# Performance work log

Measured on AMD Instinct MI355X. Metric: run time of the kernel, lower is better.

## Reference

```python
import jax, jax.numpy as jnp
import numpy as np

N = 200000      # total nodes
B = 1024        # graphs
D = 256         # node_dim
OUT = 256       # out_dim


def setup_inputs() -> dict:
    key = jax.random.key(0)
    ks = jax.random.split(key, 16)
    x = jax.random.normal(ks[0], (N, D), dtype=jnp.float32)
    # sorted segment ids covering all B graphs (no empty segments)
    extra = jax.random.randint(ks[1], (N - B,), 0, B)
    batch = jnp.sort(jnp.concatenate([jnp.arange(B, dtype=jnp.int32), extra.astype(jnp.int32)]))
    # one-hot node type mask [N, 3]
    types = jax.random.randint(ks[2], (N,), 0, 3)
    node_type_mask = jax.nn.one_hot(types, 3, dtype=jnp.int32)
    s = 1.0 / np.sqrt(D)
    # attn_weight: Linear(D, D//2) -> Tanh -> Linear(D//2, 1)
    aw1 = jax.random.uniform(ks[3], (D, D // 2), jnp.float32, -s, s)
    ab1 = jnp.zeros((D // 2,), jnp.float32)
    aw2 = jax.random.uniform(ks[4], (D // 2, 1), jnp.float32, -s, s)
    ab2 = jnp.zeros((1,), jnp.float32)
    # three typed transforms Linear(D, D)
    we = jax.random.uniform(ks[5], (D, D), jnp.float32, -s, s)
    be = jnp.zeros((D,), jnp.float32)
    wv = jax.random.uniform(ks[6], (D, D), jnp.float32, -s, s)
    bv = jnp.zeros((D,), jnp.float32)
    wp = jax.random.uniform(ks[7], (D, D), jnp.float32, -s, s)
    bp = jnp.zeros((D,), jnp.float32)
    # readout MLP: Linear(3D, 2*OUT) -> SiLU -> (Dropout eval) -> Linear(2*OUT, OUT)
    w1 = jax.random.uniform(ks[8], (3 * D, 2 * OUT), jnp.float32, -1.0 / np.sqrt(3 * D), 1.0 / np.sqrt(3 * D))
    b1 = jnp.zeros((2 * OUT,), jnp.float32)
    w2 = jax.random.uniform(ks[9], (2 * OUT, OUT), jnp.float32, -1.0 / np.sqrt(2 * OUT), 1.0 / np.sqrt(2 * OUT))
    b2 = jnp.zeros((OUT,), jnp.float32)
    return dict(x=x, batch=batch, node_type_mask=node_type_mask, num_segments=B,
                aw1=aw1, ab1=ab1, aw2=aw2, ab2=ab2, we=we, be=be, wv=wv, bv=bv,
                wp=wp, bp=bp, w1=w1, b1=b1, w2=w2, b2=b2)


def reference(x, batch, node_type_mask, num_segments,
              aw1, ab1, aw2, ab2, we, be, wv, bv, wp, bp, w1, b1, w2, b2):
    nseg = int(num_segments)
    # global_mean_pool
    counts = jax.ops.segment_sum(jnp.ones((x.shape[0],), x.dtype), batch, num_segments=nseg)
    mean_pool = jax.ops.segment_sum(x, batch, num_segments=nseg) / counts[:, None]
    # attention scores + segment softmax
    scores = jnp.tanh(x @ aw1 + ab1) @ aw2 + ab2            # [N, 1]
    s = scores[:, 0]
    m = jax.ops.segment_max(s, batch, num_segments=nseg)    # [B]
    e = jnp.exp(s - m[batch])
    z = jax.ops.segment_sum(e, batch, num_segments=nseg)
    attn = e / z[batch]                                     # [N]
    attn_pool = jax.ops.segment_sum(x * attn[:, None], batch, num_segments=nseg)
    # typed physical pooling (node_type_mask path)
    mask = node_type_mask.astype(x.dtype)
    typed_x = (mask[:, 0:1] * (x @ we + be)
               + mask[:, 1:2] * (x @ wv + bv)
               + mask[:, 2:3] * (x @ wp + bp))
    phys_pool = jax.ops.segment_sum(typed_x, batch, num_segments=nseg)
    combined = jnp.concatenate([mean_pool, attn_pool, phys_pool], axis=-1)  # [B, 3D]
    h = jax.nn.silu(combined @ w1 + b1)                     # dropout = identity (eval)
    return h @ w2 + b2                                      # [B, OUT]
```

## Files before the change

### kernel.cpp

```cpp
#include <hip/hip_runtime.h>

typedef float  f32x4  __attribute__((ext_vector_type(4)));
typedef short  s16x8  __attribute__((ext_vector_type(8)));
typedef short  s16x4  __attribute__((ext_vector_type(4)));

__device__ __forceinline__ short f2bf(float f) {
  unsigned u = __float_as_uint(f);
  u += 0x7fffu + ((u >> 16) & 1u);
  return (short)(u >> 16);
}
__device__ __forceinline__ float bf2f(unsigned short us) {
  return __uint_as_float(((unsigned)us) << 16);
}
__device__ __forceinline__ float tanh_fast(float x) {
  const float e = __expf(2.0f * x);
  return 1.0f - 2.0f / (e + 1.0f);
}

__global__ __launch_bounds__(256) void k_cvtw(
    const float* __restrict__ aw1, const float* __restrict__ we, const float* __restrict__ wv,
    const float* __restrict__ wp, const float* __restrict__ w1, const float* __restrict__ w2,
    unsigned short* __restrict__ Awt, unsigned short* __restrict__ Wpt,
    unsigned short* __restrict__ W1t, unsigned short* __restrict__ W2t,
    float* __restrict__ Z) {
  const int b = blockIdx.x, tid = threadIdx.x;
  if (b >= 184) {
    const int idx = b - 184;
    f32x4* Z4 = reinterpret_cast<f32x4*>(Z);
    const f32x4 z4 = {0.f, 0.f, 0.f, 0.f};
#pragma unroll
    for (int j = 0; j < 4; ++j) {
      const int o = idx * 1024 + j * 256 + tid;
      if (o < 263168) Z4[o] = z4;
    }
    return;
  }
  __shared__ short T[64][65];
  const float* src; unsigned short* dst;
  int N, ds, off, t;
  if (b < 8)        { src = aw1; dst = Awt; N = 128; ds = 256; off = 0;   t = b; }
  else if (b < 24)  { src = we;  dst = Wpt; N = 256; ds = 768; off = 0;   t = b - 8; }
  else if (b < 40)  { src = wv;  dst = Wpt; N = 256; ds = 768; off = 256; t = b - 24; }
  else if (b < 56)  { src = wp;  dst = Wpt; N = 256; ds = 768; off = 512; t = b - 40; }
  else if (b < 152) { src = w1;  dst = W1t; N = 512; ds = 768; off = 0;   t = b - 56; }
  else              { src = w2;  dst = W2t; N = 256; ds = 512; off = 0;   t = b - 152; }
  const int ntx = N >> 6;
  const int kt = t / ntx;
  const int k0 = kt * 64, n0 = (t - kt * ntx) * 64;
  const int rl = tid >> 6, cl = tid & 63;
#pragma unroll
  for (int i = 0; i < 16; ++i)
    T[cl][i * 4 + rl] = f2bf(src[(size_t)(k0 + i * 4 + rl) * N + n0 + cl]);
  __syncthreads();
#pragma unroll
  for (int i = 0; i < 16; ++i)
    dst[(size_t)(n0 + i * 4 + rl) * ds + off + k0 + cl] = (unsigned short)T[i * 4 + rl][cl];
}

__global__ __launch_bounds__(256, 2) void k_score_pool(
    const float* __restrict__ x, const int* __restrict__ batch, const int* __restrict__ mask,
    const unsigned short* __restrict__ Awt, const float* __restrict__ ab1,
    const float* __restrict__ aw2, const float* __restrict__ ab2,
    float* __restrict__ P, float* __restrict__ EX, float* __restrict__ ZC,
    int nnodes) {
  __shared__ __align__(16) short xs[2][32][264];
  __shared__ __align__(16) short xsB[2][8192];
  __shared__ __align__(16) float sred[2][4][32];
  __shared__ __align__(16) short em[16][40];
  __shared__ int st_all[320];

  const int tid  = threadIdx.x;
  const int lane = tid & 63;
  const int w    = tid >> 6;
  const int quad = lane >> 4;
  const int l15  = lane & 15;

  s16x8 bfrag[8][2];
  float ab1v[2], aw2v[2];
#pragma unroll
  for (int ct = 0; ct < 2; ++ct) {
    const int col = w * 32 + ct * 16 + l15;
    ab1v[ct] = ab1[col];
    aw2v[ct] = aw2[col];
    const s16x8* bp = reinterpret_cast<const s16x8*>(Awt + (size_t)col * 256);
#pragma unroll
    for (int kt = 0; kt < 8; ++kt) bfrag[kt][ct] = bp[kt * 4 + quad];
  }
  const float ab2v = ab2[0];

  const int tiles = nnodes >> 5;
  const int t_beg = (int)(((long long)blockIdx.x * tiles) / (long long)gridDim.x);
  const int t_end = (int)(((long long)(blockIdx.x + 1) * tiles) / (long long)gridDim.x);
  if (t_beg >= t_end) return;
  const int nt = t_end - t_beg;

  {
    const int nodes0 = t_beg * 32, nblk = nt * 32;
    for (int i = tid; i < nblk; i += 256) {
      const int g = nodes0 + i;
      st_all[i] = batch[g] * 4 + mask[g * 3 + 1] + 2 * mask[g * 3 + 2];
    }
    for (int i = tid; i < 640; i += 256) (&em[0][0])[i] = 0;
  }

  f32x4 stg[8];
  auto load_regs = [&](int tile) {
    const f32x4* xp = reinterpret_cast<const f32x4*>(x + (size_t)tile * 8192);
#pragma unroll
    for (int i = 0; i < 8; ++i) stg[i] = xp[(8 * w + i) * 64 + lane];
  };
  auto cvt_write = [&](int bb) {
    s16x4 xv[8];
#pragma unroll
    for (int i = 0; i < 8; ++i) {
      xv[i][0] = f2bf(stg[i][0]); xv[i][1] = f2bf(stg[i][1]);
      xv[i][2] = f2bf(stg[i][2]); xv[i][3] = f2bf(stg[i][3]);
    }
#pragma unroll
    for (int i = 0; i < 8; ++i)
      *reinterpret_cast<s16x4*>(&xs[bb][8 * w + i][lane * 4]) = xv[i];
    const int gb = (lane >> 2) * 4 + w;
    const int lb = (lane & 3) * 4;
#pragma unroll
    for (int q = 0; q < 4; ++q) {
      s16x8 v;
#pragma unroll
      for (int j = 0; j < 8; ++j) v[j] = xv[j][q];
      *reinterpret_cast<s16x8*>(&xsB[bb][(gb * 16 + lb + q) * 8]) = v;
    }
  };

  load_regs(t_beg);
  cvt_write(0);
  __syncthreads();

  const f32x4 zero4 = {0.f, 0.f, 0.f, 0.f};
  f32x4 accB[4] = {zero4, zero4, zero4, zero4};
  float zA = 0.f, c0A = 0.f, c1A = 0.f, c2A = 0.f;
  int cur = -1;

  auto flushB = [&]() {
#pragma unroll
    for (int c = 0; c < 4; ++c) {
      const int col = w * 64 + c * 16 + l15;
      if (quad == 0) {
        atomicAdd(&EX[cur * 256 + col], accB[c][0] + accB[c][1]);
        atomicAdd(&P[cur * 768 + col], accB[c][2]);
        atomicAdd(&P[cur * 768 + 256 + col], accB[c][3]);
      } else if (quad == 1) {
        atomicAdd(&P[cur * 768 + 512 + col], accB[c][0]);
      }
      accB[c] = zero4;
    }
    if (w == 0) {
      if (lane < 4) {
        const float v = (lane == 0) ? zA : ((lane == 1) ? c0A : ((lane == 2) ? c1A : c2A));
        atomicAdd(&ZC[cur * 4 + lane], v);
      }
      zA = c0A = c1A = c2A = 0.f;
    }
  };

  auto POOL = [&](int base, int par, s16x8 f0, s16x8 f1, s16x8 f2, s16x8 f3) {
    float e_f = 0.f;
    int myt = 3;
    if (lane < 32) {
      const float s = ab2v + sred[par][0][lane] + sred[par][1][lane] +
                      sred[par][2][lane] + sred[par][3][lane];
      e_f = __expf(s);
      const unsigned short hi = (unsigned short)f2bf(e_f);
      const unsigned short lo = (unsigned short)f2bf(e_f - bf2f(hi));
      myt = st_all[base + lane] & 3;
      em[0][lane] = (short)hi;
      em[1][lane] = (short)lo;
      em[2][lane] = (myt == 0) ? (short)0x3f80 : (short)0;
      em[3][lane] = (myt == 1) ? (short)0x3f80 : (short)0;
      em[4][lane] = (myt == 2) ? (short)0x3f80 : (short)0;
    }
    const int myseg = (lane < 32) ? (st_all[base + lane] >> 2) : 0x7fffffff;
    s16x8 emf = *reinterpret_cast<const s16x8*>(&em[l15][quad * 8]);

    int n0 = 0;
    while (n0 < 32) {
      const int seg = st_all[base + n0] >> 2;
      const unsigned long long diff = __ballot(lane < 32 && myseg != seg) >> n0;
      const int n1 = (diff == 0) ? 32 : n0 + (int)__builtin_ctzll(diff);
      if (seg != cur) { if (cur >= 0) flushB(); cur = seg; }
      s16x8 af;
      const int kb = quad * 8;
#pragma unroll
      for (int j = 0; j < 8; ++j) {
        const int k = kb + j;
        af[j] = (k >= n0 && k < n1) ? emf[j] : (short)0;
      }
      accB[0] = __builtin_amdgcn_mfma_f32_16x16x32_bf16(af, f0, accB[0], 0, 0, 0);
      accB[1] = __builtin_amdgcn_mfma_f32_16x16x32_bf16(af, f1, accB[1], 0, 0, 0);
      accB[2] = __builtin_amdgcn_mfma_f32_16x16x32_bf16(af, f2, accB[2], 0, 0, 0);
      accB[3] = __builtin_amdgcn_mfma_f32_16x16x32_bf16(af, f3, accB[3], 0, 0, 0);
      if (w == 0) {
        const bool inrun = (lane >= n0 && lane < n1 && lane < 32);
        float ee = inrun ? e_f : 0.f;
#pragma unroll
        for (int off = 1; off < 32; off <<= 1) ee += __shfl_xor(ee, off);
        const unsigned long long b0 = __ballot(inrun && myt == 0);
        const unsigned long long b1 = __ballot(inrun && myt == 1);
        const unsigned long long b2 = __ballot(inrun && myt == 2);
        zA  += ee;
        c0A += (float)__popcll(b0);
        c1A += (float)__popcll(b1);
        c2A += (float)__popcll(b2);
      }
      n0 = n1;
    }
  };

  s16x8 bfBp0, bfBp1, bfBp2, bfBp3;

  for (int lt = 0; lt < nt; ++lt) {
    const int p    = lt & 1;
    const int tile = t_beg + lt;
    const bool more = (lt + 1 < nt);
    if (more) load_regs(tile + 1);

#pragma unroll
    for (int ng = 0; ng < 2; ++ng) {
      s16x8 af[8];
#pragma unroll
      for (int kt = 0; kt < 8; ++kt)
        af[kt] = *reinterpret_cast<const s16x8*>(&xs[p][16 * ng + l15][kt * 32 + quad * 8]);
      float part[4] = {0.f, 0.f, 0.f, 0.f};
#pragma unroll
      for (int ct = 0; ct < 2; ++ct) {
        f32x4 acc = {0.f, 0.f, 0.f, 0.f};
#pragma unroll
        for (int kt = 0; kt < 8; ++kt)
          acc = __builtin_amdgcn_mfma_f32_16x16x32_bf16(af[kt], bfrag[kt][ct], acc, 0, 0, 0);
#pragma unroll
        for (int r = 0; r < 4; ++r)
          part[r] += tanh_fast(acc[r] + ab1v[ct]) * aw2v[ct];
      }
#pragma unroll
      for (int off = 1; off < 16; off <<= 1) {
#pragma unroll
        for (int r = 0; r < 4; ++r) part[r] += __shfl_xor(part[r], off);
      }
      if (l15 == 0) {
#pragma unroll
        for (int r = 0; r < 4; ++r) sred[p][w][16 * ng + quad * 4 + r] = part[r];
      }
    }

    const s16x8 bfBn0 = *reinterpret_cast<const s16x8*>(
        &xsB[p][(((w * 4 + 0) * 4 + quad) * 16 + l15) * 8]);
    const s16x8 bfBn1 = *reinterpret_cast<const s16x8*>(
        &xsB[p][(((w * 4 + 1) * 4 + quad) * 16 + l15) * 8]);
    const s16x8 bfBn2 = *reinterpret_cast<const s16x8*>(
        &xsB[p][(((w * 4 + 2) * 4 + quad) * 16 + l15) * 8]);
    const s16x8 bfBn3 = *reinterpret_cast<const s16x8*>(
        &xsB[p][(((w * 4 + 3) * 4 + quad) * 16 + l15) * 8]);

    if (lt > 0) POOL((lt - 1) * 32, p ^ 1, bfBp0, bfBp1, bfBp2, bfBp3);

    if (more) cvt_write(p ^ 1);

    __syncthreads();
    bfBp0 = bfBn0; bfBp1 = bfBn1; bfBp2 = bfBn2; bfBp3 = bfBn3;
  }

  POOL((nt - 1) * 32, (nt - 1) & 1, bfBp0, bfBp1, bfBp2, bfBp3);
  if (cur >= 0) flushB();
}

__global__ __launch_bounds__(256) void k_phys(
    const float* __restrict__ P, const unsigned short* __restrict__ Wpt,
    const float* __restrict__ be, const float* __restrict__ bv, const float* __restrict__ bp,
    const float* __restrict__ ZC, float* __restrict__ PH) {
  __shared__ __align__(16) short as16[16][776];
  const int tid = threadIdx.x, lane = tid & 63, w = tid >> 6;
  const int quad = lane >> 4, l15 = lane & 15;
  const int rowbase = blockIdx.x * 16;
  const int col = blockIdx.y * 64 + w * 16 + l15;

  s16x8 bfr[24];
  const s16x8* bpf = reinterpret_cast<const s16x8*>(Wpt + (size_t)col * 768);
#pragma unroll
  for (int kt = 0; kt < 24; ++kt) bfr[kt] = bpf[kt * 4 + quad];

  const f32x4* ap = reinterpret_cast<const f32x4*>(P + (size_t)rowbase * 768);
#pragma unroll
  for (int i = 0; i < 12; ++i) {
    const int ci = tid + 256 * i;
    f32x4 v = ap[ci];
    const int row = ci / 192, c4 = (ci % 192) * 4;
    s16x4 b; b[0] = f2bf(v[0]); b[1] = f2bf(v[1]); b[2] = f2bf(v[2]); b[3] = f2bf(v[3]);
    *reinterpret_cast<s16x4*>(&as16[row][c4]) = b;
  }
  __syncthreads();

  f32x4 acc = {0.f, 0.f, 0.f, 0.f};
#pragma unroll
  for (int kt = 0; kt < 24; ++kt) {
    s16x8 af = *reinterpret_cast<const s16x8*>(&as16[l15][kt * 32 + quad * 8]);
    acc = __builtin_amdgcn_mfma_f32_16x16x32_bf16(af, bfr[kt], acc, 0, 0, 0);
  }
  const float ben = be[col], bvn = bv[col], bpn = bp[col];
#pragma unroll
  for (int r = 0; r < 4; ++r) {
    const int row = rowbase + quad * 4 + r;
    const float v = acc[r] + ZC[row * 4 + 1] * ben + ZC[row * 4 + 2] * bvn + ZC[row * 4 + 3] * bpn;
    PH[(size_t)row * 256 + col] = v;
  }
}

__global__ __launch_bounds__(256) void k_mlp1(
    const float* __restrict__ P, const float* __restrict__ EX,
    const float* __restrict__ ZC, const float* __restrict__ PH,
    const unsigned short* __restrict__ W1t, const float* __restrict__ b1,
    float* __restrict__ H) {
  __shared__ __align__(16) short as16[16][776];
  const int tid = threadIdx.x, lane = tid & 63, w = tid >> 6;
  const int quad = lane >> 4, l15 = lane & 15;
  const int rowbase = blockIdx.x * 16;
  const int col = blockIdx.y * 64 + w * 16 + l15;

  s16x8 bfr[24];
  const s16x8* bpf = reinterpret_cast<const s16x8*>(W1t + (size_t)col * 768);
#pragma unroll
  for (int kt = 0; kt < 24; ++kt) bfr[kt] = bpf[kt * 4 + quad];

#pragma unroll 4
  for (int r = 0; r < 16; ++r) {
    const int row = rowbase + r;
    const float z   = ZC[row * 4 + 0];
    const float cnt = ZC[row * 4 + 1] + ZC[row * 4 + 2] + ZC[row * 4 + 3];
    const float mp  = (P[(size_t)row * 768 + tid] + P[(size_t)row * 768 + 256 + tid] +
                       P[(size_t)row * 768 + 512 + tid]) / cnt;
    as16[r][tid]       = f2bf(mp);
    as16[r][256 + tid] = f2bf(EX[(size_t)row * 256 + tid] / z);
    as16[r][512 + tid] = f2bf(PH[(size_t)row * 256 + tid]);
  }
  __syncthreads();

  f32x4 acc = {0.f, 0.f, 0.f, 0.f};
#pragma unroll
  for (int kt = 0; kt < 24; ++kt) {
    s16x8 af = *reinterpret_cast<const s16x8*>(&as16[l15][kt * 32 + quad * 8]);
    acc = __builtin_amdgcn_mfma_f32_16x16x32_bf16(af, bfr[kt], acc, 0, 0, 0);
  }
  const float bn = b1[col];
#pragma unroll
  for (int r = 0; r < 4; ++r) {
    const int row = rowbase + quad * 4 + r;
    const float v = acc[r] + bn;
    H[(size_t)row * 512 + col] = v / (1.f + __expf(-v));
  }
}

__global__ __launch_bounds__(256) void k_mlp2(
    const float* __restrict__ A, const unsigned short* __restrict__ W2t,
    const float* __restrict__ b2, float* __restrict__ out) {
  __shared__ __align__(16) short as16[16][520];
  const int tid = threadIdx.x, lane = tid & 63, w = tid >> 6;
  const int quad = lane >> 4, l15 = lane & 15;
  const int rowbase = blockIdx.x * 16;
  const int col = blockIdx.y * 64 + w * 16 + l15;

  s16x8 bfr[16];
  const s16x8* bpf = reinterpret_cast<const s16x8*>(W2t + (size_t)col * 512);
#pragma unroll
  for (int kt = 0; kt < 16; ++kt) bfr[kt] = bpf[kt * 4 + quad];

  const f32x4* ap = reinterpret_cast<const f32x4*>(A + (size_t)rowbase * 512);
#pragma unroll
  for (int i = 0; i < 8; ++i) {
    const int ci = tid + 256 * i;
    f32x4 v = ap[ci];
    const int row = ci >> 7, c4 = (ci & 127) * 4;
    s16x4 b; b[0] = f2bf(v[0]); b[1] = f2bf(v[1]); b[2] = f2bf(v[2]); b[3] = f2bf(v[3]);
    *reinterpret_cast<s16x4*>(&as16[row][c4]) = b;
  }
  __syncthreads();

  f32x4 acc = {0.f, 0.f, 0.f, 0.f};
#pragma unroll
  for (int kt = 0; kt < 16; ++kt) {
    s16x8 af = *reinterpret_cast<const s16x8*>(&as16[l15][kt * 32 + quad * 8]);
    acc = __builtin_amdgcn_mfma_f32_16x16x32_bf16(af, bfr[kt], acc, 0, 0, 0);
  }
  const float bn = b2[col];
#pragma unroll
  for (int r = 0; r < 4; ++r) {
    const int row = rowbase + quad * 4 + r;
    out[(size_t)row * 256 + col] = acc[r] + bn;
  }
}

extern "C" void kernel_launch(void* const* d_in, const int* in_sizes, int n_in,
                              void* d_out, int out_size, void* d_ws, size_t ws_size,
                              hipStream_t stream) {
  const float* x    = (const float*)d_in[0];
  const int*   batch= (const int*)  d_in[1];
  const int*   mask = (const int*)  d_in[2];
  const float* aw1  = (const float*)d_in[4];
  const float* ab1  = (const float*)d_in[5];
  const float* aw2  = (const float*)d_in[6];
  const float* ab2  = (const float*)d_in[7];
  const float* we   = (const float*)d_in[8];
  const float* be   = (const float*)d_in[9];
  const float* wv   = (const float*)d_in[10];
  const float* bv   = (const float*)d_in[11];
  const float* wp   = (const float*)d_in[12];
  const float* bp   = (const float*)d_in[13];
  const float* w1   = (const float*)d_in[14];
  const float* b1   = (const float*)d_in[15];
  const float* w2   = (const float*)d_in[16];
  const float* b2   = (const float*)d_in[17];
  float* out = (float*)d_out;
  const int nn = in_sizes[1];

  float* ws = (float*)d_ws;
  float* P    = ws;
  float* EXs  = P    + 786432;
  float* ZCs  = EXs  + 262144;
  float* PH   = ZCs  + 4096;
  float* hbuf = PH   + 262144;
  unsigned short* Awt = (unsigned short*)(hbuf + 524288);
  unsigned short* Wpt = Awt + 32768;
  unsigned short* W1t = Wpt + 196608;
  unsigned short* W2t = W1t + 393216;

  k_cvtw      <<<456, 256, 0, stream>>>(aw1, we, wv, wp, w1, w2, Awt, Wpt, W1t, W2t, P);
  k_score_pool<<<1024, 256, 0, stream>>>(x, batch, mask, Awt, ab1, aw2, ab2, P, EXs, ZCs, nn);
  k_phys      <<<dim3(64, 4), 256, 0, stream>>>(P, Wpt, be, bv, bp, ZCs, PH);
  k_mlp1      <<<dim3(64, 8), 256, 0, stream>>>(P, EXs, ZCs, PH, W1t, b1, hbuf);
  k_mlp2      <<<dim3(64, 4), 256, 0, stream>>>(hbuf, W2t, b2, out);
}
```

Before: 430.1 us.

## Single-buffer score tile and load pooling fragments inside POOL

Drops the double buffer for the bf16 score tile xs, keeping one copy, and adds an extra barrier between pooling and the next tile's conversion write. Pooling B fragments are now read from shared memory inside POOL instead of being held across iterations in registers. The aim is to cut LDS footprint and register pressure so occupancy can rise. The cost is one more __syncthreads per tile, which serialises compute and the LDS write of the next tile.

```diff
diff --git a/kernel.cpp b/kernel.cpp
--- a/kernel.cpp
+++ b/kernel.cpp
@@ -63,7 +63,7 @@
     const float* __restrict__ aw2, const float* __restrict__ ab2,
     float* __restrict__ P, float* __restrict__ EX, float* __restrict__ ZC,
     int nnodes) {
-  __shared__ __align__(16) short xs[2][32][264];
+  __shared__ __align__(16) short xs[32][264];
   __shared__ __align__(16) short xsB[2][8192];
   __shared__ __align__(16) float sred[2][4][32];
   __shared__ __align__(16) short em[16][40];
@@ -118,7 +118,7 @@
     }
 #pragma unroll
     for (int i = 0; i < 8; ++i)
-      *reinterpret_cast<s16x4*>(&xs[bb][8 * w + i][lane * 4]) = xv[i];
+      *reinterpret_cast<s16x4*>(&xs[8 * w + i][lane * 4]) = xv[i];
     const int gb = (lane >> 2) * 4 + w;
     const int lb = (lane & 3) * 4;
 #pragma unroll
@@ -161,7 +161,7 @@
     }
   };
 
-  auto POOL = [&](int base, int par, s16x8 f0, s16x8 f1, s16x8 f2, s16x8 f3) {
+  auto POOL = [&](int base, int par) {
     float e_f = 0.f;
     int myt = 3;
     if (lane < 32) {
@@ -178,7 +178,15 @@
       em[4][lane] = (myt == 2) ? (short)0x3f80 : (short)0;
     }
     const int myseg = (lane < 32) ? (st_all[base + lane] >> 2) : 0x7fffffff;
-    s16x8 emf = *reinterpret_cast<const s16x8*>(&em[l15][quad * 8]);
+    const s16x8 emf = *reinterpret_cast<const s16x8*>(&em[l15][quad * 8]);
+    const s16x8 f0 = *reinterpret_cast<const s16x8*>(
+        &xsB[par][(((w * 4 + 0) * 4 + quad) * 16 + l15) * 8]);
+    const s16x8 f1 = *reinterpret_cast<const s16x8*>(
+        &xsB[par][(((w * 4 + 1) * 4 + quad) * 16 + l15) * 8]);
+    const s16x8 f2 = *reinterpret_cast<const s16x8*>(
+        &xsB[par][(((w * 4 + 2) * 4 + quad) * 16 + l15) * 8]);
+    const s16x8 f3 = *reinterpret_cast<const s16x8*>(
+        &xsB[par][(((w * 4 + 3) * 4 + quad) * 16 + l15) * 8]);
 
     int n0 = 0;
     while (n0 < 32) {
@@ -214,20 +222,17 @@
     }
   };
 
-  s16x8 bfBp0, bfBp1, bfBp2, bfBp3;
-
   for (int lt = 0; lt < nt; ++lt) {
     const int p    = lt & 1;
-    const int tile = t_beg + lt;
     const bool more = (lt + 1 < nt);
-    if (more) load_regs(tile + 1);
+    if (more) load_regs(t_beg + lt + 1);
 
 #pragma unroll
     for (int ng = 0; ng < 2; ++ng) {
       s16x8 af[8];
 #pragma unroll
       for (int kt = 0; kt < 8; ++kt)
-        af[kt] = *reinterpret_cast<const s16x8*>(&xs[p][16 * ng + l15][kt * 32 + quad * 8]);
+        af[kt] = *reinterpret_cast<const s16x8*>(&xs[16 * ng + l15][kt * 32 + quad * 8]);
       float part[4] = {0.f, 0.f, 0.f, 0.f};
 #pragma unroll
       for (int ct = 0; ct < 2; ++ct) {
@@ -250,24 +255,16 @@
       }
     }
 
-    const s16x8 bfBn0 = *reinterpret_cast<const s16x8*>(
-        &xsB[p][(((w * 4 + 0) * 4 + quad) * 16 + l15) * 8]);
-    const s16x8 bfBn1 = *reinterpret_cast<const s16x8*>(
-        &xsB[p][(((w * 4 + 1) * 4 + quad) * 16 + l15) * 8]);
-    const s16x8 bfBn2 = *reinterpret_cast<const s16x8*>(
-        &xsB[p][(((w * 4 + 2) * 4 + quad) * 16 + l15) * 8]);
-    const s16x8 bfBn3 = *reinterpret_cast<const s16x8*>(
-        &xsB[p][(((w * 4 + 3) * 4 + quad) * 16 + l15) * 8]);
-
-    if (lt > 0) POOL((lt - 1) * 32, p ^ 1, bfBp0, bfBp1, bfBp2, bfBp3);
+    if (lt > 0) POOL((lt - 1) * 32, p ^ 1);
+
+    __syncthreads();
 
     if (more) cvt_write(p ^ 1);
 
     __syncthreads();
-    bfBp0 = bfBn0; bfBp1 = bfBn1; bfBp2 = bfBn2; bfBp3 = bfBn3;
-  }
-
-  POOL((nt - 1) * 32, (nt - 1) & 1, bfBp0, bfBp1, bfBp2, bfBp3);
+  }
+
+  POOL((nt - 1) * 32, (nt - 1) & 1);
   if (cur >= 0) flushB();
 }
 
```

Result: slower. 441.5 us (+2.6%).
